# Optimization experiments

Hardware: AMD Instinct MI355X
Metric: run time of the kernel (lower is better)

## Reference

```python
import jax, jax.numpy as jnp
import numpy as np

N_NODES = 4096
N_EDGES = 500000
N_PAIRS = 2000000
EDGE_DIM = 16
MAX_PATH = 5


def setup_inputs() -> dict:
    key = jax.random.key(0)
    k1, k2, k3, k4, k5 = jax.random.split(key, 5)
    x = jax.random.normal(k1, (N_NODES, EDGE_DIM), dtype=jnp.float32)
    edge_attr = jax.random.normal(k2, (N_EDGES, EDGE_DIM), dtype=jnp.float32)
    path_idx = jax.random.randint(k3, (N_PAIRS, MAX_PATH), 0, N_EDGES, dtype=jnp.int64)
    path_lens = jax.random.randint(k4, (N_PAIRS,), 0, MAX_PATH + 1, dtype=jnp.int64)
    pair_id = jnp.arange(N_PAIRS, dtype=jnp.int64)
    # learned parameter: edge_weights [max_path_distance, edge_dim]
    edge_weights = jax.random.normal(k5, (MAX_PATH, EDGE_DIM), dtype=jnp.float32)
    return {"x": x, "edge_attr": edge_attr, "edge_weights": edge_weights,
            "path_idx": path_idx, "path_lens": path_lens, "pair_id": pair_id}


def reference(x, edge_attr, edge_weights, path_idx, path_lens, pair_id):
    N = x.shape[0]
    L = edge_weights.shape[0]  # max_path_distance
    # valid-position mask for each ragged path, padded to length L
    mask = (jnp.arange(L)[None, :] < path_lens[:, None]).astype(edge_attr.dtype)  # [P, L]
    gathered = edge_attr[path_idx]  # [P, L, D] ragged gather of edge features
    # per-hop dot with learned per-hop weight vector, i.e. (w_l * e_l).sum(dim=1)
    dots = jnp.einsum('pld,ld->pl', gathered, edge_weights)  # [P, L]
    s = jnp.sum(dots * mask, axis=1)  # [P]
    cnt = path_lens.astype(edge_attr.dtype)
    # mean over valid hops; empty path -> NaN in torch -> nan_to_num -> 0
    mean = jnp.where(cnt > 0, s / jnp.maximum(cnt, 1.0), jnp.zeros_like(s))
    src = pair_id % N
    dst = pair_id // N  # unique (src, dst) pairs by construction
    cij = jnp.zeros((N, N), dtype=edge_attr.dtype).at[src, dst].set(mean)
    return cij
```

## Files before the change

### kernel.cpp

```cpp
#include <hip/hip_runtime.h>
#include <hip/hip_fp16.h>

#define NNODES 4096
#define NEDGES 500000
#define NPAIRS 2000000
#define EDIM   16
#define LMAX   5

typedef int v4i __attribute__((ext_vector_type(4)));

__device__ __forceinline__ v4i ntload4(const int* p) {
  return __builtin_nontemporal_load((const v4i*)p);
}

__global__ __launch_bounds__(256) void dots_kernel(
    const float* __restrict__ edge_attr,
    const float* __restrict__ ew,
    __half* __restrict__ dots) {
  __shared__ float w[LMAX * EDIM];
  int tid = threadIdx.x;
  if (tid < LMAX * EDIM) w[tid] = ew[tid];
  __syncthreads();

  int e0 = (blockIdx.x * 256 + tid) * 2;
  if (e0 >= NEDGES) return;

  const float4* ra = (const float4*)(edge_attr + (size_t)e0 * EDIM);
  float4 a0 = ra[0], a1 = ra[1], a2 = ra[2], a3 = ra[3];
  float4 b0 = ra[4], b1 = ra[5], b2 = ra[6], b3 = ra[7];
  float va[16] = {a0.x, a0.y, a0.z, a0.w, a1.x, a1.y, a1.z, a1.w,
                  a2.x, a2.y, a2.z, a2.w, a3.x, a3.y, a3.z, a3.w};
  float vb[16] = {b0.x, b0.y, b0.z, b0.w, b1.x, b1.y, b1.z, b1.w,
                  b2.x, b2.y, b2.z, b2.w, b3.x, b3.y, b3.z, b3.w};
#pragma unroll
  for (int l = 0; l < LMAX; ++l) {
    float da = 0.f, db = 0.f;
#pragma unroll
    for (int k = 0; k < EDIM; ++k) {
      da += va[k] * w[l * EDIM + k];
      db += vb[k] * w[l * EDIM + k];
    }
    __half2 h;
    h.x = __float2half(da);
    h.y = __float2half(db);
    *(__half2*)(dots + (size_t)l * NEDGES + e0) = h;
  }
}

__device__ __forceinline__ float pair_mean(
    const __half* __restrict__ dots, int len,
    int i0, int i1, int i2, int i3, int i4) {
  len = min(max(len, 0), LMAX);
  float v0 = (len > 0) ? __half2float(dots[i0]) : 0.f;
  float v1 = (len > 1) ? __half2float(dots[1 * NEDGES + i1]) : 0.f;
  float v2 = (len > 2) ? __half2float(dots[2 * NEDGES + i2]) : 0.f;
  float v3 = (len > 3) ? __half2float(dots[3 * NEDGES + i3]) : 0.f;
  float v4 = (len > 4) ? __half2float(dots[4 * NEDGES + i4]) : 0.f;
  float s = ((v0 + v1) + (v2 + v3)) + v4;
  return (len > 0) ? s / (float)len : 0.f;
}

__global__ __launch_bounds__(256) void fused_mean_transpose(
    const int* __restrict__ path_idx,
    const int* __restrict__ path_lens,
    const __half* __restrict__ dots,
    float* __restrict__ out) {
  const int src0 = blockIdx.x * 64;
  const int dst0 = blockIdx.y * 64;
  const int tid = threadIdx.x;

  if (dst0 * NNODES >= NPAIRS) {
    float4 z = {0.f, 0.f, 0.f, 0.f};
#pragma unroll
    for (int i = 0; i < 4; ++i) {
      int slot = tid + i * 256;
      int a = slot >> 4;
      int c = slot & 15;
      ((float4*)(out + (size_t)(src0 + a) * NNODES + dst0))[c] = z;
    }
    return;
  }

  __shared__ float tile[64][65];

#pragma unroll
  for (int i = 0; i < 4; ++i) {
    int slot = tid + i * 256;
    int a = slot >> 4;
    int c = slot & 15;
    int p = (dst0 + a) * NNODES + src0 + 4 * c;
    float4 v = {0.f, 0.f, 0.f, 0.f};
    if (p < NPAIRS) {
      v4i ln = ntload4(path_lens + p);
      const int* q = path_idx + (size_t)p * LMAX;
      v4i A = ntload4(q);
      v4i B = ntload4(q + 4);
      v4i C = ntload4(q + 8);
      v4i D = ntload4(q + 12);
      v4i E = ntload4(q + 16);
      v.x = pair_mean(dots, ln[0], A[0], A[1], A[2], A[3], B[0]);
      v.y = pair_mean(dots, ln[1], B[1], B[2], B[3], C[0], C[1]);
      v.z = pair_mean(dots, ln[2], C[2], C[3], D[0], D[1], D[2]);
      v.w = pair_mean(dots, ln[3], D[3], E[0], E[1], E[2], E[3]);
    }
    tile[a][4 * c + 0] = v.x;
    tile[a][4 * c + 1] = v.y;
    tile[a][4 * c + 2] = v.z;
    tile[a][4 * c + 3] = v.w;
  }
  __syncthreads();
#pragma unroll
  for (int i = 0; i < 4; ++i) {
    int slot = tid + i * 256;
    int a = slot >> 4;
    int c = slot & 15;
    float4 v;
    v.x = tile[4 * c + 0][a];
    v.y = tile[4 * c + 1][a];
    v.z = tile[4 * c + 2][a];
    v.w = tile[4 * c + 3][a];
    ((float4*)(out + (size_t)(src0 + a) * NNODES + dst0))[c] = v;
  }
}

__global__ __launch_bounds__(256) void scatter_kernel(
    const float* __restrict__ edge_attr,
    const float* __restrict__ ew,
    const int* __restrict__ path_idx,
    const int* __restrict__ path_lens,
    float* __restrict__ out) {
  __shared__ float w[LMAX * EDIM];
  if (threadIdx.x < LMAX * EDIM) w[threadIdx.x] = ew[threadIdx.x];
  __syncthreads();

  int p = blockIdx.x * 256 + threadIdx.x;
  if (p >= NPAIRS) return;

  int len = path_lens[p];
  len = min(max(len, 0), LMAX);

  const int* row = path_idx + (size_t)p * LMAX;
  float s = 0.f;
  for (int l = 0; l < len; ++l) {
    int idx = row[l];
    const float4* r = (const float4*)(edge_attr + (size_t)idx * EDIM);
    float4 a0 = r[0], a1 = r[1], a2 = r[2], a3 = r[3];
    const float* wl = &w[l * EDIM];
    s += a0.x * wl[0] + a0.y * wl[1] + a0.z * wl[2] + a0.w * wl[3] +
         a1.x * wl[4] + a1.y * wl[5] + a1.z * wl[6] + a1.w * wl[7] +
         a2.x * wl[8] + a2.y * wl[9] + a2.z * wl[10] + a2.w * wl[11] +
         a3.x * wl[12] + a3.y * wl[13] + a3.z * wl[14] + a3.w * wl[15];
  }
  float m = (len > 0) ? (s / (float)len) : 0.f;
  int src = p & (NNODES - 1);
  int dst = p >> 12;
  out[(size_t)src * NNODES + dst] = m;
}

extern "C" void kernel_launch(void* const* d_in, const int* in_sizes, int n_in,
                              void* d_out, int out_size, void* d_ws, size_t ws_size,
                              hipStream_t stream) {
  const float* edge_attr = (const float*)d_in[1];
  const float* edge_w    = (const float*)d_in[2];
  const int*   path_idx  = (const int*)d_in[3];
  const int*   path_lens = (const int*)d_in[4];
  float* out = (float*)d_out;

  const size_t need = (size_t)LMAX * NEDGES * sizeof(__half);

  if (ws_size >= need) {
    __half* dots = (__half*)d_ws;

    dots_kernel<<<(NEDGES / 2 + 255) / 256, 256, 0, stream>>>(edge_attr, edge_w, dots);
    dim3 grid(64, 64), block(256, 1);
    fused_mean_transpose<<<grid, block, 0, stream>>>(path_idx, path_lens, dots, out);
  } else {
    hipMemsetAsync(d_out, 0, (size_t)out_size * sizeof(float), stream);
    scatter_kernel<<<(NPAIRS + 255) / 256, 256, 0, stream>>>(
        edge_attr, edge_w, path_idx, path_lens, out);
  }
}
```

Measured before the change: 179.4 us.

## Interleave heavy and zero-fill tiles in a 1D grid with 1024-thread blocks and nontemporal stores

The 2D grid becomes a 1D grid in which the first 1024 blocks alternate between compute tiles (the dst tiles that hold pairs) and zero-fill tiles, so heavy and light work share the GPU from the start. The remaining blocks only zero-fill. Each block now has 1024 threads, so every thread handles one float4 slot and the per-thread loops go away. Output writes use nontemporal stores to avoid polluting the cache. The risks are larger blocks giving coarser scheduling, and the hand-written block index mapping covering the tiles incorrectly.

After: 217.2 us. +21.1%, slower.

```diff
diff --git a/kernel.cpp b/kernel.cpp
--- a/kernel.cpp
+++ b/kernel.cpp
@@ -8,9 +8,14 @@
 #define LMAX   5
 
 typedef int v4i __attribute__((ext_vector_type(4)));
+typedef float v4f __attribute__((ext_vector_type(4)));
 
 __device__ __forceinline__ v4i ntload4(const int* p) {
   return __builtin_nontemporal_load((const v4i*)p);
+}
+__device__ __forceinline__ void ntstore4(float* p, float x, float y, float z, float w) {
+  v4f t = {x, y, z, w};
+  __builtin_nontemporal_store(t, (v4f*)p);
 }
 
 __global__ __launch_bounds__(256) void dots_kernel(
@@ -60,34 +65,39 @@
   return (len > 0) ? s / (float)len : 0.f;
 }
 
-__global__ __launch_bounds__(256) void fused_mean_transpose(
+__global__ __launch_bounds__(1024) void fused_mean_transpose(
     const int* __restrict__ path_idx,
     const int* __restrict__ path_lens,
     const __half* __restrict__ dots,
     float* __restrict__ out) {
-  const int src0 = blockIdx.x * 64;
-  const int dst0 = blockIdx.y * 64;
+  int bid = blockIdx.x;
+  int dst_t, src_t;
+  bool heavy;
+  if (bid < 1024) {
+    heavy = (bid & 1);
+    int k = bid >> 1;
+    if (heavy) { dst_t = k & 7;        src_t = k >> 3; }
+    else       { dst_t = 8 + (k >> 6); src_t = k & 63; }
+  } else {
+    heavy = false;
+    int z = bid - 512;
+    dst_t = 8 + (z >> 6);
+    src_t = z & 63;
+  }
+  const int src0 = src_t * 64;
+  const int dst0 = dst_t * 64;
   const int tid = threadIdx.x;
+  const int a = tid >> 4;
+  const int c = tid & 15;
 
-  if (dst0 * NNODES >= NPAIRS) {
-    float4 z = {0.f, 0.f, 0.f, 0.f};
-#pragma unroll
-    for (int i = 0; i < 4; ++i) {
-      int slot = tid + i * 256;
-      int a = slot >> 4;
-      int c = slot & 15;
-      ((float4*)(out + (size_t)(src0 + a) * NNODES + dst0))[c] = z;
-    }
+  if (!heavy) {
+    ntstore4(out + (size_t)(src0 + a) * NNODES + dst0 + 4 * c, 0.f, 0.f, 0.f, 0.f);
     return;
   }
 
   __shared__ float tile[64][65];
 
-#pragma unroll
-  for (int i = 0; i < 4; ++i) {
-    int slot = tid + i * 256;
-    int a = slot >> 4;
-    int c = slot & 15;
+  {
     int p = (dst0 + a) * NNODES + src0 + 4 * c;
     float4 v = {0.f, 0.f, 0.f, 0.f};
     if (p < NPAIRS) {
@@ -109,17 +119,12 @@
     tile[a][4 * c + 3] = v.w;
   }
   __syncthreads();
-#pragma unroll
-  for (int i = 0; i < 4; ++i) {
-    int slot = tid + i * 256;
-    int a = slot >> 4;
-    int c = slot & 15;
-    float4 v;
-    v.x = tile[4 * c + 0][a];
-    v.y = tile[4 * c + 1][a];
-    v.z = tile[4 * c + 2][a];
-    v.w = tile[4 * c + 3][a];
-    ((float4*)(out + (size_t)(src0 + a) * NNODES + dst0))[c] = v;
+  {
+    float x = tile[4 * c + 0][a];
+    float y = tile[4 * c + 1][a];
+    float z = tile[4 * c + 2][a];
+    float w = tile[4 * c + 3][a];
+    ntstore4(out + (size_t)(src0 + a) * NNODES + dst0 + 4 * c, x, y, z, w);
   }
 }
 
@@ -172,8 +177,7 @@
     __half* dots = (__half*)d_ws;
 
     dots_kernel<<<(NEDGES / 2 + 255) / 256, 256, 0, stream>>>(edge_attr, edge_w, dots);
-    dim3 grid(64, 64), block(256, 1);
-    fused_mean_transpose<<<grid, block, 0, stream>>>(path_idx, path_lens, dots, out);
+    fused_mean_transpose<<<4096, 1024, 0, stream>>>(path_idx, path_lens, dots, out);
   } else {
     hipMemsetAsync(d_out, 0, (size_t)out_size * sizeof(float), stream);
     scatter_kernel<<<(NPAIRS + 255) / 256, 256, 0, stream>>>(
```
